# Kernel tuning notes

Measured on AMD Instinct MI355X. Metric: run time of the kernel, lower is better.

Reference implementation:

```python
import jax, jax.numpy as jnp
import numpy as np

N_NODES = 50000
N_EDGES = 800000
IN_DIM = 8
HID = 32
HEADS = 4
D1 = HID * HEADS  # 128


def setup_inputs() -> dict:
    key = jax.random.key(0)
    ks = jax.random.split(key, 10)
    x = jax.random.normal(ks[0], (N_NODES, IN_DIM), dtype=jnp.float32)
    edge_index = jax.random.randint(ks[1], (2, N_EDGES), 0, N_NODES, dtype=jnp.int64)
    s = lambda fan_in: 1.0 / np.sqrt(fan_in)
    W1 = jax.random.uniform(ks[2], (IN_DIM, D1), jnp.float32, -s(IN_DIM), s(IN_DIM))
    a1 = jax.random.uniform(ks[3], (2 * D1, 1), jnp.float32, -s(2 * D1), s(2 * D1))
    W2 = jax.random.uniform(ks[4], (D1, HID), jnp.float32, -s(D1), s(D1))
    a2 = jax.random.uniform(ks[5], (2 * HID, 1), jnp.float32, -s(2 * HID), s(2 * HID))
    hw1 = jax.random.uniform(ks[6], (HID, 32), jnp.float32, -s(HID), s(HID))
    hb1 = jax.random.uniform(ks[7], (32,), jnp.float32, -s(HID), s(HID))
    hw2 = jax.random.uniform(ks[8], (32, 1), jnp.float32, -s(32), s(32))
    hb2 = jax.random.uniform(ks[9], (1,), jnp.float32, -s(32), s(32))
    return {"x": x, "edge_index": edge_index, "W1": W1, "a1": a1,
            "W2": W2, "a2": a2, "hw1": hw1, "hb1": hb1, "hw2": hw2, "hb2": hb2}


def gat_layer(h, src, dst, W, a, n_nodes):
    # Wh: [N, D]; attention vector split so logits are computed per-node then gathered
    Wh = h @ W
    D = Wh.shape[-1]
    a_src, a_dst = a[:D, 0], a[D:, 0]
    # alpha = LeakyReLU([Wh[src] || Wh[dst]] @ a)  (same math, no [E, 2D] concat)
    alpha = jax.nn.leaky_relu((Wh @ a_src)[src] + (Wh @ a_dst)[dst], negative_slope=0.2)
    alpha_exp = jnp.exp(alpha - alpha.max())  # global-max shift, as in the original
    alpha_sum = jax.ops.segment_sum(alpha_exp, dst, num_segments=n_nodes)
    alpha_norm = alpha_exp / (alpha_sum[dst] + 1e-9)
    out = jax.ops.segment_sum(alpha_norm[:, None] * Wh[src], dst, num_segments=n_nodes)
    return jax.nn.elu(out), alpha_norm


def reference(x, edge_index, W1, a1, W2, a2, hw1, hb1, hw2, hb2):
    src, dst = edge_index[0], edge_index[1]
    n = x.shape[0]
    h, _ = gat_layer(x, src, dst, W1, a1, n)
    h, _ = gat_layer(h, src, dst, W2, a2, n)
    # head: Linear -> GELU -> (Dropout: identity in eval) -> Linear
    z = jax.nn.gelu(h @ hw1 + hb1, approximate=False)
    node_scores = (z @ hw2 + hb2).squeeze(-1)
    return node_scores
```

## Files before the change

kernel.cpp:

```cpp
#include <hip/hip_runtime.h>
#include <math.h>

#define N_NODES 50000
#define IN_DIM 8
#define HID 32
#define D1 128

#define CAP 64

#define FG 8
#define FB 128
#define GRANGE (N_NODES / FG)
#define FILL_BLOCKS (FG * FB)
#define SD1_BLOCKS ((N_NODES + 255) / 256)

__global__ void k_fill_sd1(const int* __restrict__ src, const int* __restrict__ dst,
                           int* __restrict__ cnt, int* __restrict__ esrc,
                           const float* __restrict__ x, const float* __restrict__ W1,
                           const float* __restrict__ a1,
                           float* __restrict__ s1, float* __restrict__ d1,
                           int n_edges) {
    __shared__ float bs[IN_DIM], bd[IN_DIM];
    const int t = threadIdx.x;
    if (blockIdx.x < FILL_BLOCKS) {
        const int g = blockIdx.x & (FG - 1);
        const int blk = blockIdx.x >> 3;
        const int lo = g * GRANGE, hi = lo + GRANGE;
        const int base = blk * blockDim.x + t;
        const int step = FB * blockDim.x;
        for (int i = base; i * 4 < n_edges; i += step) {
            const int4 d4 = *(const int4*)&dst[i * 4];
            const bool mx = d4.x >= lo && d4.x < hi;
            const bool my = d4.y >= lo && d4.y < hi;
            const bool mz = d4.z >= lo && d4.z < hi;
            const bool mw = d4.w >= lo && d4.w < hi;
            if (mx | my | mz | mw) {
                const int4 s4 = *(const int4*)&src[i * 4];
                if (mx) { const int p = atomicAdd(&cnt[d4.x], 1); if (p < CAP) esrc[d4.x * CAP + p] = s4.x; }
                if (my) { const int p = atomicAdd(&cnt[d4.y], 1); if (p < CAP) esrc[d4.y * CAP + p] = s4.y; }
                if (mz) { const int p = atomicAdd(&cnt[d4.z], 1); if (p < CAP) esrc[d4.z * CAP + p] = s4.z; }
                if (mw) { const int p = atomicAdd(&cnt[d4.w], 1); if (p < CAP) esrc[d4.w * CAP + p] = s4.w; }
            }
        }
    } else {
        if (t < 16) {
            const int k = t & 7;
            const float* av = a1 + ((t < 8) ? 0 : D1);
            float acc = 0.f;
            for (int j = 0; j < D1; ++j) acc += W1[k * D1 + j] * av[j];
            if (t < 8) bs[k] = acc; else bd[k] = acc;
        }
        __syncthreads();
        const int node = (blockIdx.x - FILL_BLOCKS) * blockDim.x + t;
        if (node >= N_NODES) return;
        const float4 x0 = *(const float4*)&x[node * 8];
        const float4 x1 = *(const float4*)&x[node * 8 + 4];
        s1[node] = x0.x*bs[0] + x0.y*bs[1] + x0.z*bs[2] + x0.w*bs[3]
                 + x1.x*bs[4] + x1.y*bs[5] + x1.z*bs[6] + x1.w*bs[7];
        d1[node] = x0.x*bd[0] + x0.y*bd[1] + x0.z*bd[2] + x0.w*bd[3]
                 + x1.x*bd[4] + x1.y*bd[5] + x1.z*bd[6] + x1.w*bd[7];
    }
}

__global__ void k_aggr_mid(const int* __restrict__ esrc, const int* __restrict__ cnt,
                           const float* __restrict__ s, const float* __restrict__ d,
                           const float* __restrict__ x,
                           const float* __restrict__ W1, const float* __restrict__ W2,
                           const float* __restrict__ a2,
                           float* __restrict__ Wh2,
                           float* __restrict__ s2, float* __restrict__ d2) {
    __shared__ float xa_s[8][IN_DIM];
    __shared__ float h_s[8][D1];
    const int t = threadIdx.x;
    const int wv = t >> 6;
    const int lane = t & 63;
    const int half = lane >> 5, sub = lane & 31;
    const int nodeBase = blockIdx.x * 8;
    const int node = nodeBase + wv * 2 + half;
    const int start = node * CAP;
    const int deg = cnt[node];
    const float dn = d[node];
    float4 aLo = {0.f, 0.f, 0.f, 0.f};
    float4 aHi = {0.f, 0.f, 0.f, 0.f};
    float wsum = 0.f;
    for (int idx = sub; idx < deg; idx += 32) {
        const int se = esrc[start + idx];
        float a = s[se] + dn;
        a = a > 0.f ? a : 0.2f * a;
        const float ww = expf(a);
        const float4 v0 = *(const float4*)&x[se * IN_DIM];
        const float4 v1 = *(const float4*)&x[se * IN_DIM + 4];
        aLo.x += ww * v0.x;  aLo.y += ww * v0.y;
        aLo.z += ww * v0.z;  aLo.w += ww * v0.w;
        aHi.x += ww * v1.x;  aHi.y += ww * v1.y;
        aHi.z += ww * v1.z;  aHi.w += ww * v1.w;
        wsum += ww;
    }
#pragma unroll
    for (int off = 1; off < 32; off <<= 1) {
        aLo.x += __shfl_xor(aLo.x, off);
        aLo.y += __shfl_xor(aLo.y, off);
        aLo.z += __shfl_xor(aLo.z, off);
        aLo.w += __shfl_xor(aLo.w, off);
        aHi.x += __shfl_xor(aHi.x, off);
        aHi.y += __shfl_xor(aHi.y, off);
        aHi.z += __shfl_xor(aHi.z, off);
        aHi.w += __shfl_xor(aHi.w, off);
        wsum  += __shfl_xor(wsum, off);
    }
    const float inv = 1.f / (wsum + 1e-9f);
    if (sub == 0) {
        float4 o; o.x = aLo.x*inv; o.y = aLo.y*inv; o.z = aLo.z*inv; o.w = aLo.w*inv;
        *(float4*)&xa_s[wv * 2 + half][0] = o;
    } else if (sub == 1) {
        float4 o; o.x = aHi.x*inv; o.y = aHi.y*inv; o.z = aHi.z*inv; o.w = aHi.w*inv;
        *(float4*)&xa_s[wv * 2 + half][4] = o;
    }
    __syncthreads();
    const int nloc = t >> 5;
    const int col = t & 31;
    const float xa0 = xa_s[nloc][0], xa1 = xa_s[nloc][1];
    const float xa2 = xa_s[nloc][2], xa3 = xa_s[nloc][3];
    const float xa4 = xa_s[nloc][4], xa5 = xa_s[nloc][5];
    const float xa6 = xa_s[nloc][6], xa7 = xa_s[nloc][7];
#pragma unroll
    for (int j = 0; j < 4; ++j) {
        const int k = col + 32 * j;
        float h = xa0 * W1[0 * D1 + k] + xa1 * W1[1 * D1 + k]
                + xa2 * W1[2 * D1 + k] + xa3 * W1[3 * D1 + k]
                + xa4 * W1[4 * D1 + k] + xa5 * W1[5 * D1 + k]
                + xa6 * W1[6 * D1 + k] + xa7 * W1[7 * D1 + k];
        h_s[nloc][k] = h > 0.f ? h : (expf(h) - 1.f);
    }
    __syncthreads();
    float o = 0.f;
#pragma unroll 8
    for (int k = 0; k < D1; ++k) o += h_s[nloc][k] * W2[k * HID + col];
    float ss = o * a2[col];
    float dd = o * a2[HID + col];
#pragma unroll
    for (int off = 1; off < 32; off <<= 1) {
        ss += __shfl_xor(ss, off);
        dd += __shfl_xor(dd, off);
    }
    const int node2 = nodeBase + nloc;
    Wh2[node2 * HID + col] = o;
    if (col == 0) { s2[node2] = ss; d2[node2] = dd; }
}

__global__ void k_aggr32_head(const int* __restrict__ esrc, const int* __restrict__ cnt,
                              const float* __restrict__ s, const float* __restrict__ d,
                              const float* __restrict__ Wh,
                              const float* __restrict__ hw1, const float* __restrict__ hb1,
                              const float* __restrict__ hw2, const float* __restrict__ hb2,
                              float* __restrict__ scores) {
    const int w = (blockIdx.x * blockDim.x + threadIdx.x) >> 6;
    const int lane = threadIdx.x & 63;
    const int half = lane >> 5, sub = lane & 31, base = lane & 32;
    const int node = w * 2 + half;
    if (node >= N_NODES) return;
    const int start = node * CAP;
    const int deg = cnt[node];
    const float dn = d[node];
    const int slot = sub >> 3;
    const int cp = sub & 7;
    float4 acc = {0.f, 0.f, 0.f, 0.f};
    float wsum = 0.f;
    for (int idx = slot; idx < deg; idx += 4) {
        const int se = esrc[start + idx];
        float a = s[se] + dn;
        a = a > 0.f ? a : 0.2f * a;
        const float ww = expf(a);
        const float4 v = *(const float4*)&Wh[se * HID + cp * 4];
        acc.x += ww * v.x;  acc.y += ww * v.y;
        acc.z += ww * v.z;  acc.w += ww * v.w;
        wsum += ww;
    }
#pragma unroll
    for (int off = 8; off < 32; off <<= 1) {
        acc.x += __shfl_xor(acc.x, off);
        acc.y += __shfl_xor(acc.y, off);
        acc.z += __shfl_xor(acc.z, off);
        acc.w += __shfl_xor(acc.w, off);
        wsum  += __shfl_xor(wsum, off);
    }
    const float inv = 1.f / (wsum + 1e-9f);
    acc.x *= inv;  acc.y *= inv;  acc.z *= inv;  acc.w *= inv;
    const int srcl = base + (sub >> 2);
    const float g0 = __shfl(acc.x, srcl);
    const float g1 = __shfl(acc.y, srcl);
    const float g2 = __shfl(acc.z, srcl);
    const float g3 = __shfl(acc.w, srcl);
    const int r = sub & 3;
    float v = (r == 0) ? g0 : (r == 1) ? g1 : (r == 2) ? g2 : g3;
    const float h = v > 0.f ? v : (expf(v) - 1.f);
    float z = hb1[sub];
#pragma unroll
    for (int k = 0; k < HID; ++k) {
        const float hk = __shfl(h, base + k);
        z += hk * hw1[k * HID + sub];
    }
    z = 0.5f * z * (1.f + erff(z * 0.7071067811865475f));
    float sc = z * hw2[sub];
#pragma unroll
    for (int off = 16; off > 0; off >>= 1) sc += __shfl_xor(sc, off);
    if (sub == 0) scores[node] = sc + hb2[0];
}

extern "C" void kernel_launch(void* const* d_in, const int* in_sizes, int n_in,
                              void* d_out, int out_size, void* d_ws, size_t ws_size,
                              hipStream_t stream) {
    const float* x   = (const float*)d_in[0];
    const int*   ei  = (const int*)d_in[1];
    const float* W1  = (const float*)d_in[2];
    const float* a1  = (const float*)d_in[3];
    const float* W2  = (const float*)d_in[4];
    const float* a2  = (const float*)d_in[5];
    const float* hw1 = (const float*)d_in[6];
    const float* hb1 = (const float*)d_in[7];
    const float* hw2 = (const float*)d_in[8];
    const float* hb2 = (const float*)d_in[9];
    float* out = (float*)d_out;

    const int n_edges = in_sizes[1] / 2;
    const int* src = ei;
    const int* dst = ei + n_edges;

    float* p = (float*)d_ws;
    float* Wh2  = p; p += (size_t)N_NODES * HID;
    float* s1   = p; p += N_NODES;
    float* d1   = p; p += N_NODES;
    float* s2   = p; p += N_NODES;
    float* d2   = p; p += N_NODES;
    int* cnt    = (int*)p; p += N_NODES;
    int* esrc   = (int*)p; p += (size_t)N_NODES * CAP;

    hipMemsetAsync(cnt, 0, N_NODES * sizeof(int), stream);

    const int AGGR_BLOCKS = (N_NODES * 32 + 255) / 256;

    k_fill_sd1<<<FILL_BLOCKS + SD1_BLOCKS, 256, 0, stream>>>(
        src, dst, cnt, esrc, x, W1, a1, s1, d1, n_edges);

    k_aggr_mid<<<(N_NODES + 7) / 8, 256, 0, stream>>>(esrc, cnt, s1, d1, x,
                                                      W1, W2, a2, Wh2, s2, d2);

    k_aggr32_head<<<AGGR_BLOCKS, 256, 0, stream>>>(esrc, cnt, s2, d2, Wh2,
                                                   hw1, hb1, hw2, hb2, out);
}
```

Measured before the change: 180.6 us.

## Inline bucket counts with edge lists and pack node features with logit

Merges the per-node count into slot 0 of each 64-int bucket record, so the count and the edge list share a cache line. It also packs x and the layer-1 source logit into a 16-float per-node record, so each gathered neighbour needs one line instead of two separate loads. In exchange, the memset now clears the whole bucket array (about 12.8 MB instead of 200 KB), per-node capacity drops to 63 edges, and the packed records use twice the footprint of x.

Result: slower. 232.5 us (+28.7%).

```diff
diff --git a/kernel.cpp b/kernel.cpp
--- a/kernel.cpp
+++ b/kernel.cpp
@@ -6,7 +6,8 @@
 #define HID 32
 #define D1 128
 
-#define CAP 64
+#define REC 64
+#define CAPE 63
 
 #define FG 8
 #define FB 128
@@ -15,10 +16,10 @@
 #define SD1_BLOCKS ((N_NODES + 255) / 256)
 
 __global__ void k_fill_sd1(const int* __restrict__ src, const int* __restrict__ dst,
-                           int* __restrict__ cnt, int* __restrict__ esrc,
+                           int* __restrict__ bkt,
                            const float* __restrict__ x, const float* __restrict__ W1,
                            const float* __restrict__ a1,
-                           float* __restrict__ s1, float* __restrict__ d1,
+                           float* __restrict__ px, float* __restrict__ d1,
                            int n_edges) {
     __shared__ float bs[IN_DIM], bd[IN_DIM];
     const int t = threadIdx.x;
@@ -36,10 +37,10 @@
             const bool mw = d4.w >= lo && d4.w < hi;
             if (mx | my | mz | mw) {
                 const int4 s4 = *(const int4*)&src[i * 4];
-                if (mx) { const int p = atomicAdd(&cnt[d4.x], 1); if (p < CAP) esrc[d4.x * CAP + p] = s4.x; }
-                if (my) { const int p = atomicAdd(&cnt[d4.y], 1); if (p < CAP) esrc[d4.y * CAP + p] = s4.y; }
-                if (mz) { const int p = atomicAdd(&cnt[d4.z], 1); if (p < CAP) esrc[d4.z * CAP + p] = s4.z; }
-                if (mw) { const int p = atomicAdd(&cnt[d4.w], 1); if (p < CAP) esrc[d4.w * CAP + p] = s4.w; }
+                if (mx) { const int p = atomicAdd(&bkt[d4.x * REC], 1); if (p < CAPE) bkt[d4.x * REC + 1 + p] = s4.x; }
+                if (my) { const int p = atomicAdd(&bkt[d4.y * REC], 1); if (p < CAPE) bkt[d4.y * REC + 1 + p] = s4.y; }
+                if (mz) { const int p = atomicAdd(&bkt[d4.z * REC], 1); if (p < CAPE) bkt[d4.z * REC + 1 + p] = s4.z; }
+                if (mw) { const int p = atomicAdd(&bkt[d4.w * REC], 1); if (p < CAPE) bkt[d4.w * REC + 1 + p] = s4.w; }
             }
         }
     } else {
@@ -55,16 +56,18 @@
         if (node >= N_NODES) return;
         const float4 x0 = *(const float4*)&x[node * 8];
         const float4 x1 = *(const float4*)&x[node * 8 + 4];
-        s1[node] = x0.x*bs[0] + x0.y*bs[1] + x0.z*bs[2] + x0.w*bs[3]
-                 + x1.x*bs[4] + x1.y*bs[5] + x1.z*bs[6] + x1.w*bs[7];
-        d1[node] = x0.x*bd[0] + x0.y*bd[1] + x0.z*bd[2] + x0.w*bd[3]
-                 + x1.x*bd[4] + x1.y*bd[5] + x1.z*bd[6] + x1.w*bd[7];
-    }
-}
-
-__global__ void k_aggr_mid(const int* __restrict__ esrc, const int* __restrict__ cnt,
-                           const float* __restrict__ s, const float* __restrict__ d,
-                           const float* __restrict__ x,
+        const float s1v = x0.x*bs[0] + x0.y*bs[1] + x0.z*bs[2] + x0.w*bs[3]
+                        + x1.x*bs[4] + x1.y*bs[5] + x1.z*bs[6] + x1.w*bs[7];
+        d1[node]       = x0.x*bd[0] + x0.y*bd[1] + x0.z*bd[2] + x0.w*bd[3]
+                        + x1.x*bd[4] + x1.y*bd[5] + x1.z*bd[6] + x1.w*bd[7];
+        *(float4*)&px[node * 16]     = x0;
+        *(float4*)&px[node * 16 + 4] = x1;
+        px[node * 16 + 8] = s1v;
+    }
+}
+
+__global__ void k_aggr_mid(const int* __restrict__ bkt,
+                           const float* __restrict__ px, const float* __restrict__ d,
                            const float* __restrict__ W1, const float* __restrict__ W2,
                            const float* __restrict__ a2,
                            float* __restrict__ Wh2,
@@ -77,19 +80,20 @@
     const int half = lane >> 5, sub = lane & 31;
     const int nodeBase = blockIdx.x * 8;
     const int node = nodeBase + wv * 2 + half;
-    const int start = node * CAP;
-    const int deg = cnt[node];
+    const int rec = node * REC;
+    const int deg = bkt[rec];
     const float dn = d[node];
     float4 aLo = {0.f, 0.f, 0.f, 0.f};
     float4 aHi = {0.f, 0.f, 0.f, 0.f};
     float wsum = 0.f;
     for (int idx = sub; idx < deg; idx += 32) {
-        const int se = esrc[start + idx];
-        float a = s[se] + dn;
+        const int se = bkt[rec + 1 + idx];
+        const float4 v0 = *(const float4*)&px[se * 16];
+        const float4 v1 = *(const float4*)&px[se * 16 + 4];
+        const float sv = px[se * 16 + 8];
+        float a = sv + dn;
         a = a > 0.f ? a : 0.2f * a;
         const float ww = expf(a);
-        const float4 v0 = *(const float4*)&x[se * IN_DIM];
-        const float4 v1 = *(const float4*)&x[se * IN_DIM + 4];
         aLo.x += ww * v0.x;  aLo.y += ww * v0.y;
         aLo.z += ww * v0.z;  aLo.w += ww * v0.w;
         aHi.x += ww * v1.x;  aHi.y += ww * v1.y;
@@ -148,7 +152,7 @@
     if (col == 0) { s2[node2] = ss; d2[node2] = dd; }
 }
 
-__global__ void k_aggr32_head(const int* __restrict__ esrc, const int* __restrict__ cnt,
+__global__ void k_aggr32_head(const int* __restrict__ bkt,
                               const float* __restrict__ s, const float* __restrict__ d,
                               const float* __restrict__ Wh,
                               const float* __restrict__ hw1, const float* __restrict__ hb1,
@@ -159,15 +163,15 @@
     const int half = lane >> 5, sub = lane & 31, base = lane & 32;
     const int node = w * 2 + half;
     if (node >= N_NODES) return;
-    const int start = node * CAP;
-    const int deg = cnt[node];
+    const int rec = node * REC;
+    const int deg = bkt[rec];
     const float dn = d[node];
     const int slot = sub >> 3;
     const int cp = sub & 7;
     float4 acc = {0.f, 0.f, 0.f, 0.f};
     float wsum = 0.f;
     for (int idx = slot; idx < deg; idx += 4) {
-        const int se = esrc[start + idx];
+        const int se = bkt[rec + 1 + idx];
         float a = s[se] + dn;
         a = a > 0.f ? a : 0.2f * a;
         const float ww = expf(a);
@@ -227,24 +231,23 @@
     const int* dst = ei + n_edges;
 
     float* p = (float*)d_ws;
+    float* px   = p; p += (size_t)N_NODES * 16;
     float* Wh2  = p; p += (size_t)N_NODES * HID;
-    float* s1   = p; p += N_NODES;
     float* d1   = p; p += N_NODES;
     float* s2   = p; p += N_NODES;
     float* d2   = p; p += N_NODES;
-    int* cnt    = (int*)p; p += N_NODES;
-    int* esrc   = (int*)p; p += (size_t)N_NODES * CAP;
-
-    hipMemsetAsync(cnt, 0, N_NODES * sizeof(int), stream);
+    int* bkt    = (int*)p; p += (size_t)N_NODES * REC;
+
+    hipMemsetAsync(bkt, 0, (size_t)N_NODES * REC * sizeof(int), stream);
 
     const int AGGR_BLOCKS = (N_NODES * 32 + 255) / 256;
 
     k_fill_sd1<<<FILL_BLOCKS + SD1_BLOCKS, 256, 0, stream>>>(
-        src, dst, cnt, esrc, x, W1, a1, s1, d1, n_edges);
-
-    k_aggr_mid<<<(N_NODES + 7) / 8, 256, 0, stream>>>(esrc, cnt, s1, d1, x,
+        src, dst, bkt, x, W1, a1, px, d1, n_edges);
+
+    k_aggr_mid<<<(N_NODES + 7) / 8, 256, 0, stream>>>(bkt, px, d1,
                                                       W1, W2, a2, Wh2, s2, d2);
 
-    k_aggr32_head<<<AGGR_BLOCKS, 256, 0, stream>>>(esrc, cnt, s2, d2, Wh2,
+    k_aggr32_head<<<AGGR_BLOCKS, 256, 0, stream>>>(bkt, s2, d2, Wh2,
                                                    hw1, hb1, hw2, hb2, out);
 }
```

## Assign one wavefront per node in layer-2 aggregation with 32 edge slots

Applied to the files above, without the earlier changes.

The final aggregation+head kernel now maps one 64-lane wavefront to each node instead of half a wavefront. Each lane pair handles one edge, with each lane loading 16 channels, so up to 32 edges are processed in parallel rather than 4. This is meant to cut the serial edge-loop length and expose more memory-level parallelism for the gathers. In exchange it doubles the launched threads, adds a 5-step butterfly reduction over 17 values, and leaves most lanes idle for low-degree nodes (average degree is about 16).

Measured after the change: 221.8 us. +22.8%, slower.

```diff
diff --git a/kernel.cpp b/kernel.cpp
--- a/kernel.cpp
+++ b/kernel.cpp
@@ -154,57 +154,62 @@
                               const float* __restrict__ hw1, const float* __restrict__ hb1,
                               const float* __restrict__ hw2, const float* __restrict__ hb2,
                               float* __restrict__ scores) {
-    const int w = (blockIdx.x * blockDim.x + threadIdx.x) >> 6;
+    const int node = (blockIdx.x * blockDim.x + threadIdx.x) >> 6;
     const int lane = threadIdx.x & 63;
-    const int half = lane >> 5, sub = lane & 31, base = lane & 32;
-    const int node = w * 2 + half;
     if (node >= N_NODES) return;
     const int start = node * CAP;
     const int deg = cnt[node];
     const float dn = d[node];
-    const int slot = sub >> 3;
-    const int cp = sub & 7;
-    float4 acc = {0.f, 0.f, 0.f, 0.f};
+    const int slot = lane >> 1;
+    const int ch = lane & 1;
+    float acc[16];
+#pragma unroll
+    for (int j = 0; j < 16; ++j) acc[j] = 0.f;
     float wsum = 0.f;
-    for (int idx = slot; idx < deg; idx += 4) {
-        const int se = esrc[start + idx];
-        float a = s[se] + dn;
-        a = a > 0.f ? a : 0.2f * a;
-        const float ww = expf(a);
-        const float4 v = *(const float4*)&Wh[se * HID + cp * 4];
-        acc.x += ww * v.x;  acc.y += ww * v.y;
-        acc.z += ww * v.z;  acc.w += ww * v.w;
-        wsum += ww;
-    }
-#pragma unroll
-    for (int off = 8; off < 32; off <<= 1) {
-        acc.x += __shfl_xor(acc.x, off);
-        acc.y += __shfl_xor(acc.y, off);
-        acc.z += __shfl_xor(acc.z, off);
-        acc.w += __shfl_xor(acc.w, off);
-        wsum  += __shfl_xor(wsum, off);
+    for (int base = 0; base < deg; base += 32) {
+        const int idx = base + slot;
+        if (idx < deg) {
+            const int se = esrc[start + idx];
+            float a = s[se] + dn;
+            a = a > 0.f ? a : 0.2f * a;
+            const float ww = expf(a);
+            const float* wp = &Wh[se * HID + ch * 16];
+            const float4 v0 = *(const float4*)&wp[0];
+            const float4 v1 = *(const float4*)&wp[4];
+            const float4 v2 = *(const float4*)&wp[8];
+            const float4 v3 = *(const float4*)&wp[12];
+            acc[0]  += ww*v0.x; acc[1]  += ww*v0.y; acc[2]  += ww*v0.z; acc[3]  += ww*v0.w;
+            acc[4]  += ww*v1.x; acc[5]  += ww*v1.y; acc[6]  += ww*v1.z; acc[7]  += ww*v1.w;
+            acc[8]  += ww*v2.x; acc[9]  += ww*v2.y; acc[10] += ww*v2.z; acc[11] += ww*v2.w;
+            acc[12] += ww*v3.x; acc[13] += ww*v3.y; acc[14] += ww*v3.z; acc[15] += ww*v3.w;
+            wsum += ww;
+        }
+    }
+#pragma unroll
+    for (int off = 2; off < 64; off <<= 1) {
+#pragma unroll
+        for (int j = 0; j < 16; ++j) acc[j] += __shfl_xor(acc[j], off);
+        wsum += __shfl_xor(wsum, off);
     }
     const float inv = 1.f / (wsum + 1e-9f);
-    acc.x *= inv;  acc.y *= inv;  acc.z *= inv;  acc.w *= inv;
-    const int srcl = base + (sub >> 2);
-    const float g0 = __shfl(acc.x, srcl);
-    const float g1 = __shfl(acc.y, srcl);
-    const float g2 = __shfl(acc.z, srcl);
-    const float g3 = __shfl(acc.w, srcl);
-    const int r = sub & 3;
-    float v = (r == 0) ? g0 : (r == 1) ? g1 : (r == 2) ? g2 : g3;
-    const float h = v > 0.f ? v : (expf(v) - 1.f);
-    float z = hb1[sub];
+    float h[16];
+#pragma unroll
+    for (int j = 0; j < 16; ++j) {
+        const float v = acc[j] * inv;
+        h[j] = v > 0.f ? v : (expf(v) - 1.f);
+    }
+    const int c = lane & 31;
+    float z = hb1[c];
 #pragma unroll
     for (int k = 0; k < HID; ++k) {
-        const float hk = __shfl(h, base + k);
-        z += hk * hw1[k * HID + sub];
+        const float hk = __shfl(h[k & 15], k >> 4);
+        z += hk * hw1[k * HID + c];
     }
     z = 0.5f * z * (1.f + erff(z * 0.7071067811865475f));
-    float sc = z * hw2[sub];
-#pragma unroll
-    for (int off = 16; off > 0; off >>= 1) sc += __shfl_xor(sc, off);
-    if (sub == 0) scores[node] = sc + hb2[0];
+    float sc = z * hw2[c];
+#pragma unroll
+    for (int off = 1; off < 32; off <<= 1) sc += __shfl_xor(sc, off);
+    if (lane == 0) scores[node] = sc + hb2[0];
 }
 
 extern "C" void kernel_launch(void* const* d_in, const int* in_sizes, int n_in,
@@ -237,14 +242,12 @@
 
     hipMemsetAsync(cnt, 0, N_NODES * sizeof(int), stream);
 
-    const int AGGR_BLOCKS = (N_NODES * 32 + 255) / 256;
-
     k_fill_sd1<<<FILL_BLOCKS + SD1_BLOCKS, 256, 0, stream>>>(
         src, dst, cnt, esrc, x, W1, a1, s1, d1, n_edges);
 
     k_aggr_mid<<<(N_NODES + 7) / 8, 256, 0, stream>>>(esrc, cnt, s1, d1, x,
                                                       W1, W2, a2, Wh2, s2, d2);
 
-    k_aggr32_head<<<AGGR_BLOCKS, 256, 0, stream>>>(esrc, cnt, s2, d2, Wh2,
-                                                   hw1, hb1, hw2, hb2, out);
-}
+    k_aggr32_head<<<(N_NODES * 64 + 255) / 256, 256, 0, stream>>>(
+        esrc, cnt, s2, d2, Wh2, hw1, hb1, hw2, hb2, out);
+}
```
